# Optimization experiments

Measured on AMD Instinct MI355X. Metric: run time of the kernel, lower is better.

## Reference

```python
import jax, jax.numpy as jnp
import numpy as np
import math

RES = 1024          # FastTrigLookup / FastPhaseProcessor resolution
TWO_PI = 2.0 * math.pi
D = 512             # model dim


def setup_inputs() -> dict:
    key = jax.random.key(0)
    ks = jax.random.split(key, 4)
    B, L = 4, 4096

    def xavier(k, shape):
        fan_out, fan_in = shape
        std = math.sqrt(2.0 / (fan_in + fan_out))
        return jax.random.normal(k, shape, jnp.float32) * std

    return {
        "x": jax.random.normal(ks[0], (B, L, D), jnp.float32),
        "ft_w": xavier(ks[1], (2 * D, D)),
        "ft_b": jnp.zeros((2 * D,), jnp.float32),
        "ln_g": jnp.ones((2 * D,), jnp.float32),
        "ln_b": jnp.zeros((2 * D,), jnp.float32),
        "exc": jnp.ones((1,), jnp.float32) * 0.1,  # excitation_factor init
        "qkv_w": xavier(ks[2], (6 * D, 6 * D)),
        "qkv_b": jnp.zeros((6 * D,), jnp.float32),
        "op_w": xavier(ks[3], (2 * D, 2 * D)),
        "op_b": jnp.zeros((2 * D,), jnp.float32),
    }


def _forward(x, ft_w, ft_b, ln_g, ln_b, exc, qkv_w, qkv_b, op_w, op_b):
    B, L = x.shape[:2]
    sin_tab = jnp.sin(jnp.linspace(0.0, TWO_PI, RES)).astype(x.dtype)
    cos_tab = jnp.cos(jnp.linspace(0.0, TWO_PI, RES)).astype(x.dtype)

    # --- SimpleQuantumState: fused Linear -> tanh-GELU -> LayerNorm ---
    t = x @ ft_w.T + ft_b                                  # [B,L,2D]
    c1, c2 = 0.044715, math.sqrt(2.0 / math.pi)
    g = 0.5 * t * (1.0 + jnp.tanh(c2 * (t + c1 * t ** 3)))
    mu = g.mean(-1, keepdims=True)
    var = ((g - mu) ** 2).mean(-1, keepdims=True)
    n = (g - mu) * jax.lax.rsqrt(var + 1e-5) * ln_g + ln_b
    rp, ip = n[..., :D], n[..., D:]
    # atan2 -> gather-based sin/cos lookup (torch .long() truncates toward 0;
    # negative indices wrap from the end -> emulate with mod RES)
    ang = jnp.arctan2(ip + 1e-8, rp + 1e-8)
    idx = jnp.mod((ang / TWO_PI * (RES - 1)).astype(jnp.int32), RES)
    real = rp * cos_tab[idx]
    imag = ip * sin_tab[idx]
    nrm = jax.lax.rsqrt(real ** 2 + imag ** 2 + 1e-8) * math.sqrt(1.0 / D)
    real, imag = real * nrm, imag * nrm

    # --- EnhancedDynamicPhaseSpace: collapse prevention via trig lookup ---
    amp = jnp.sqrt(real ** 2 + imag ** 2 + 1e-8)
    coll = (amp < 0.1).astype(x.dtype)
    el = jnp.linspace(0.0, 1.0, D) * TWO_PI                # energy_levels * 2pi
    lidx = jnp.clip((jnp.mod(el, TWO_PI) / TWO_PI * RES).astype(jnp.int32), 0, RES - 1)
    real = real + coll * cos_tab[lidx] * exc
    imag = imag + coll * sin_tab[lidx] * exc
    nrm2 = jax.lax.rsqrt(real ** 2 + imag ** 2 + 1e-8)
    real, imag = real * nrm2, imag * nrm2

    # --- BasicQuantumAttention with q=k=v = quantum state (pad_mask=None) ---
    qkv_in = jnp.concatenate([real, imag, real, imag, real, imag], axis=-1)  # [B,L,6D]
    qkv = (qkv_in @ qkv_w.T + qkv_b).reshape(B, L, 6, D)
    q_r, k_r = qkv[:, :, 0], qkv[:, :, 2]
    v_r, v_i = qkv[:, :, 4], qkv[:, :, 5]
    scores = jnp.einsum('bld,bmd->blm', q_r, k_r) * (D ** -0.5)
    attn = jax.nn.softmax(scores, axis=-1)                 # dropout=eval -> identity
    o = jnp.concatenate([jnp.einsum('blm,bmd->bld', attn, v_r),
                         jnp.einsum('blm,bmd->bld', attn, v_i)], axis=-1)
    out = o @ op_w.T + op_b                                # [B,L,2D]
    return out


def reference(x, ft_w, ft_b, ln_g, ln_b, exc, qkv_w, qkv_b, op_w, op_b):
    out = _forward(x, ft_w, ft_b, ln_g, ln_b, exc, qkv_w, qkv_b, op_w, op_b)
    return (out[..., :D], out[..., D:])
```

## Files before the change

### kernel.cpp

```cpp
#include <hip/hip_runtime.h>
#include <hip/hip_bf16.h>
#include <math.h>


#define TWO_PI_F 6.283185307179586f

typedef __attribute__((ext_vector_type(4))) float f32x4;
typedef __attribute__((ext_vector_type(8))) short bf16x8;
typedef __attribute__((ext_vector_type(4))) unsigned short u16x4;
typedef __hip_bfloat16 bf16;

__device__ __forceinline__ void gl_lds16(const void* g, void* l) {
  __builtin_amdgcn_global_load_lds((const __attribute__((address_space(1))) void*)g,
                                   (__attribute__((address_space(3))) void*)l, 16, 0, 0);
}
__device__ __forceinline__ unsigned short f2bf_bits(float f) {
  union { __hip_bfloat16 h; unsigned short u; } cv;
  cv.h = __float2bfloat16(f);
  return cv.u;
}
__device__ __forceinline__ float bf_bits2f(unsigned short b) {
  union { unsigned int u; float f; } cv;
  cv.u = ((unsigned int)b) << 16;
  return cv.f;
}

template <int EPI, int ORD>
__global__ __launch_bounds__(256, 2) void gemm128(
    const bf16* __restrict__ A, const bf16* __restrict__ B, void* __restrict__ C,
    void* __restrict__ Cx, const float* __restrict__ bias, int K, int lda, int ldb, int ldc,
    float scale, long long zsa, long long zsb, long long zsc, float* __restrict__ P0,
    float* __restrict__ P1) {
  __shared__ __align__(16) bf16 sA[128 * 64];
  __shared__ __align__(16) bf16 sB[128 * 64];
  const int tid = threadIdx.x;
  const int lane = tid & 63, wid = tid >> 6;
  const int wm = wid >> 1, wn = wid & 1;

  const int gx = gridDim.x, gy = gridDim.y;
  int flat = blockIdx.x + gx * (blockIdx.y + gy * blockIdx.z);
  {
    const int nwg = gx * gy * gridDim.z;
    const int q = nwg >> 3, r = nwg & 7;
    const int x = flat & 7, loc = flat >> 3;
    flat = (x < r ? x * (q + 1) : r * (q + 1) + (x - r) * q) + loc;
  }
  const int bx = flat % gx;
  const int by = (flat / gx) % gy;
  const int bz = flat / (gx * gy);
  const int bm = by * 128, bn = bx * 128;

  const bf16 *Az, *Bz;
  if constexpr (EPI == 3) {
    const int b = bz & 1, c = bz >> 1;
    Az = A + (long long)b * zsa + c * 2048;
    Bz = B + (long long)b * zsb + c * 2048;
  } else {
    Az = A + (long long)bz * zsa;
    Bz = B + (long long)bz * zsb;
  }

  f32x4 acc[4][4];
#pragma unroll
  for (int i = 0; i < 4; ++i)
#pragma unroll
    for (int j = 0; j < 4; ++j) acc[i][j] = (f32x4){0.f, 0.f, 0.f, 0.f};

  int rowStg[4], gaStg[4];
#pragma unroll
  for (int t = 0; t < 4; ++t) {
    const int c = tid + 256 * t;
    const int r = c >> 3, s = c & 7;
    rowStg[t] = r;
    gaStg[t] = ((s ^ (r & 7)) << 3);
  }
  long long rowA[4], rowB[4];
#pragma unroll
  for (int t = 0; t < 4; ++t) {
    rowA[t] = (long long)(bm + rowStg[t]) * lda + gaStg[t];
    rowB[t] = (long long)(bn + rowStg[t]) * ldb + gaStg[t];
  }

  const int fr = lane & 15, ksl = lane >> 4;

  for (int k0 = 0; k0 < K; k0 += 64) {
#pragma unroll
    for (int t = 0; t < 4; ++t)
      gl_lds16(Az + rowA[t] + k0, &sA[(tid + 256 * t) * 8]);
#pragma unroll
    for (int t = 0; t < 4; ++t)
      gl_lds16(Bz + rowB[t] + k0, &sB[(tid + 256 * t) * 8]);
    __syncthreads();
    bf16x8 af[4][2], bfv[4][2];
#pragma unroll
    for (int i = 0; i < 4; ++i) {
      const int R = wm * 64 + i * 16 + fr;
#pragma unroll
      for (int kk = 0; kk < 2; ++kk) {
        const int s = (kk * 4 + ksl) ^ (R & 7);
        af[i][kk] = *(const bf16x8*)&sA[R * 64 + s * 8];
      }
    }
#pragma unroll
    for (int j = 0; j < 4; ++j) {
      const int R = wn * 64 + j * 16 + fr;
#pragma unroll
      for (int kk = 0; kk < 2; ++kk) {
        const int s = (kk * 4 + ksl) ^ (R & 7);
        bfv[j][kk] = *(const bf16x8*)&sB[R * 64 + s * 8];
      }
    }
#pragma unroll
    for (int kk = 0; kk < 2; ++kk)
#pragma unroll
      for (int i = 0; i < 4; ++i)
#pragma unroll
        for (int j = 0; j < 4; ++j) {
          if constexpr (ORD == 0)
            acc[i][j] =
                __builtin_amdgcn_mfma_f32_16x16x32_bf16(af[i][kk], bfv[j][kk], acc[i][j], 0, 0, 0);
          else
            acc[i][j] =
                __builtin_amdgcn_mfma_f32_16x16x32_bf16(bfv[j][kk], af[i][kk], acc[i][j], 0, 0, 0);
        }
    __syncthreads();
  }

#pragma unroll
  for (int i = 0; i < 4; ++i)
#pragma unroll
    for (int j = 0; j < 4; ++j) {
      if constexpr (ORD == 1) {
        const int row = bm + wm * 64 + i * 16 + fr;
        const int col0 = bn + wn * 64 + j * 16 + ksl * 4;
        f32x4 v = acc[i][j];
#pragma unroll
        for (int r = 0; r < 4; ++r) v[r] *= scale;
        if constexpr (EPI == 0 || EPI == 1) {
          if (bias) {
            const f32x4 bv = *(const f32x4*)&bias[col0];
            v += bv;
          }
        }
        if constexpr (EPI == 1) {
#pragma unroll
          for (int r = 0; r < 4; ++r) {
            const float t = v[r];
            float y = 0.7978845608028654f * (t + 0.044715f * t * t * t);
            y = fminf(fmaxf(y, -15.f), 15.f);
            const float e = __expf(2.f * y);
            v[r] = t * e / (1.f + e);
          }
        }
        if constexpr (EPI == 3) {
          const int b = bz & 1, c = bz >> 1;
          if (c == 0) {
            const f32x4 bv = *(const f32x4*)&bias[col0];
            v += bv;
            float* dst = (col0 < 512) ? (float*)C : (float*)Cx;
            const long long rout = zsc + (long long)b * 4096 + row;
            *(f32x4*)&dst[rout * 512 + (col0 & 511)] = v;
          } else {
            float* dst = b ? P1 : P0;
            *(f32x4*)&dst[(long long)row * 1024 + col0] = v;
          }
        } else if constexpr (EPI == 2) {
          bf16* cc = (bf16*)C + (long long)bz * zsc;
          u16x4 w;
#pragma unroll
          for (int r = 0; r < 4; ++r) w[r] = f2bf_bits(v[r]);
          *(u16x4*)&cc[(long long)row * ldc + col0] = w;
        } else {
          bf16* cc = (bf16*)C;
          u16x4 w;
#pragma unroll
          for (int r = 0; r < 4; ++r) w[r] = f2bf_bits(v[r]);
          *(u16x4*)&cc[(long long)row * ldc + col0] = w;
        }
      } else {
        const int row0 = bm + wm * 64 + i * 16 + ksl * 4;
        const int d = bn + wn * 64 + j * 16 + fr;
        u16x4 w;
#pragma unroll
        for (int r = 0; r < 4; ++r) w[r] = f2bf_bits(acc[i][j][r] * scale + bias[d]);
        const int b = row0 >> 12, mm = row0 & 4095;
        *(u16x4*)((unsigned short*)Cx + ((long long)(b * 1024 + d)) * 4096 + mm) = w;
      }
    }
  (void)ldc;
}

__global__ __launch_bounds__(256) void combine_kernel(const float* __restrict__ p0,
                                                      const float* __restrict__ p1,
                                                      float* __restrict__ out0,
                                                      float* __restrict__ out1) {
  const int idx = blockIdx.x * 256 + threadIdx.x;
  const int b = idx >> 20;
  const int rem = idx & 1048575;
  const int row = rem >> 8;
  const int c4 = rem & 255;
  const float* p = b ? p1 : p0;
  const f32x4 v = *(const f32x4*)(p + (long long)row * 1024 + c4 * 4);
  float* dst = (c4 < 128) ? out0 : out1;
  const long long o = ((long long)(b * 4096 + row)) * 512 + (c4 & 127) * 4;
  f32x4 d = *(f32x4*)(dst + o);
  d += v;
  *(f32x4*)(dst + o) = d;
}

__global__ __launch_bounds__(256) void ln_phase_kernel(
    const bf16* __restrict__ g, bf16* __restrict__ u, const float* __restrict__ ln_g,
    const float* __restrict__ ln_b, const float* __restrict__ lcos,
    const float* __restrict__ lsin, const float* __restrict__ cost,
    const float* __restrict__ sint) {
  __shared__ float sg[1024];
  __shared__ float red[4];
  const int tid = threadIdx.x;
  const int lane = tid & 63, wid = tid >> 6;
  const long long row = blockIdx.x;
  const bf16* gr = g + row * 1024;

  const u16x4 raw = *(const u16x4*)(gr + tid * 4);
  float lv[4];
  float lsum = 0.f;
#pragma unroll
  for (int e = 0; e < 4; ++e) {
    lv[e] = bf_bits2f(raw[e]);
    lsum += lv[e];
  }
  *(f32x4*)&sg[tid * 4] = *(f32x4*)lv;
#pragma unroll
  for (int off = 32; off > 0; off >>= 1) lsum += __shfl_xor(lsum, off);
  if (lane == 0) red[wid] = lsum;
  __syncthreads();
  const float mu = (red[0] + red[1] + red[2] + red[3]) * (1.0f / 1024.0f);
  __syncthreads();
  float lvar = 0.f;
#pragma unroll
  for (int e = 0; e < 4; ++e) {
    const float d = lv[e] - mu;
    lvar += d * d;
  }
#pragma unroll
  for (int off = 32; off > 0; off >>= 1) lvar += __shfl_xor(lvar, off);
  if (lane == 0) red[wid] = lvar;
  __syncthreads();
  const float var = (red[0] + red[1] + red[2] + red[3]) * (1.0f / 1024.0f);
  const float rs = rsqrtf(var + 1e-5f);

#pragma unroll
  for (int kk = 0; kk < 2; ++kk) {
    const int p = tid + kk * 256;
    const float rp = (sg[p] - mu) * rs * ln_g[p] + ln_b[p];
    const float ip = (sg[p + 512] - mu) * rs * ln_g[p + 512] + ln_b[p + 512];
    const float ang = atan2f(ip + 1e-8f, rp + 1e-8f);
    int idx = (int)((ang / TWO_PI_F) * 1023.0f);
    idx = idx < 0 ? idx + 1024 : idx;
    float real = rp * cost[idx];
    float imag = ip * sint[idx];
    const float nrm = rsqrtf(real * real + imag * imag + 1e-8f) * 0.044194173824159216f;
    real *= nrm;
    imag *= nrm;
    const float amp = sqrtf(real * real + imag * imag + 1e-8f);
    const float coll = (amp < 0.1f) ? 1.0f : 0.0f;
    real += coll * lcos[p];
    imag += coll * lsin[p];
    const float n2 = rsqrtf(real * real + imag * imag + 1e-8f);
    u[row * 1024 + p] = __float2bfloat16(real * n2);
    u[row * 1024 + 512 + p] = __float2bfloat16(imag * n2);
  }
}

__global__ __launch_bounds__(256) void softmax_kernel(bf16* __restrict__ s) {
  __shared__ float ss[4096];
  __shared__ float red[4];
  const int tid = threadIdx.x;
  const int lane = tid & 63, wid = tid >> 6;
  bf16* sr = s + (long long)blockIdx.x * 4096;
  float mx = -3.0e38f;
#pragma unroll
  for (int k = 0; k < 4; ++k) {
    const int base = (k * 256 + tid) * 4;
    const u16x4 raw = *(const u16x4*)(sr + base);
    f32x4 f;
#pragma unroll
    for (int e = 0; e < 4; ++e) {
      f[e] = bf_bits2f(raw[e]);
      mx = fmaxf(mx, f[e]);
    }
    *(f32x4*)&ss[base] = f;
  }
#pragma unroll
  for (int off = 32; off > 0; off >>= 1) mx = fmaxf(mx, __shfl_xor(mx, off));
  if (lane == 0) red[wid] = mx;
  __syncthreads();
  mx = fmaxf(fmaxf(red[0], red[1]), fmaxf(red[2], red[3]));
  __syncthreads();
  float sum = 0.f;
#pragma unroll
  for (int k = 0; k < 4; ++k) {
    const int base = (k * 256 + tid) * 4;
    f32x4 f = *(f32x4*)&ss[base];
#pragma unroll
    for (int e = 0; e < 4; ++e) {
      f[e] = __expf(f[e] - mx);
      sum += f[e];
    }
    *(f32x4*)&ss[base] = f;
  }
#pragma unroll
  for (int off = 32; off > 0; off >>= 1) sum += __shfl_xor(sum, off);
  if (lane == 0) red[wid] = sum;
  __syncthreads();
  const float inv = 1.0f / (red[0] + red[1] + red[2] + red[3]);
#pragma unroll
  for (int k = 0; k < 4; ++k) {
    const int base = (k * 256 + tid) * 4;
    const f32x4 f = *(f32x4*)&ss[base];
    u16x4 w;
#pragma unroll
    for (int e = 0; e < 4; ++e) w[e] = f2bf_bits(f[e] * inv);
    *(u16x4*)(sr + base) = w;
  }
}

__global__ __launch_bounds__(256) void fold_all(
    const float* __restrict__ w, const float* __restrict__ b,
    const float* __restrict__ op_w, const float* __restrict__ exc,
    const float* __restrict__ ft_w, const float* __restrict__ x, bf16* __restrict__ weff,
    bf16* __restrict__ wvT, float* __restrict__ beff, float* __restrict__ cost,
    float* __restrict__ sint, float* __restrict__ lcos, float* __restrict__ lsin,
    bf16* __restrict__ ftw_b, bf16* __restrict__ opw_b, bf16* __restrict__ x_b) {
  __shared__ float tile[32][33];
  __shared__ float red[4];
  const int blk = blockIdx.x;
  const int tid = threadIdx.x;
  if (blk < 4096) {
    const int i = blk * 256 + tid;
    const int o = i >> 10, j = i & 1023;
    const int so = (o < 512) ? o : o + 512;
    const float* wr = w + (long long)so * 3072;
    weff[i] = __float2bfloat16(wr[j] + wr[1024 + j] + wr[2048 + j]);
    if (j == 0) beff[o] = b[so];
  } else if (blk < 5120) {
    const int tb = blk - 4096;
    const int t0 = (tb & 31) * 32, j0 = (tb >> 5) * 32;
    const int tx = tid & 31, ty = tid >> 5;
#pragma unroll
    for (int k = 0; k < 4; ++k) {
      const int t = t0 + ty + k * 8;
      const float* wr = w + (long long)(2048 + t) * 3072 + j0 + tx;
      tile[ty + k * 8][tx] = wr[0] + wr[1024] + wr[2048];
    }
    __syncthreads();
#pragma unroll
    for (int k = 0; k < 4; ++k) {
      const int r = ty + k * 8;
      wvT[(long long)(j0 + r) * 1024 + t0 + tx] = __float2bfloat16(tile[tx][r]);
    }
  } else if (blk < 6144) {
    const int o = blk - 5120;
    const int lane = tid & 63, wid = tid >> 6;
    float s = 0.f;
#pragma unroll
    for (int k = 0; k < 4; ++k) {
      const int t = tid + k * 256;
      s += op_w[(long long)o * 1024 + t] * b[2048 + t];
    }
#pragma unroll
    for (int off = 32; off > 0; off >>= 1) s += __shfl_xor(s, off);
    if (lane == 0) red[wid] = s;
    __syncthreads();
    if (tid == 0) beff[1024 + o] = red[0] + red[1] + red[2] + red[3];
  } else if (blk == 6144) {
    const double step = 6.283185307179586 / 1023.0;
#pragma unroll
    for (int k = 0; k < 4; ++k) {
      const int i = tid + k * 256;
      const float a = (float)((double)i * step);
      cost[i] = cosf(a);
      sint[i] = sinf(a);
    }
#pragma unroll
    for (int k = 0; k < 2; ++k) {
      const int i = tid + k * 256;
      const float el = ((float)i / 511.0f) * TWO_PI_F;
      const float m = fmodf(el, TWO_PI_F);
      int li = (int)((m / TWO_PI_F) * 1024.0f);
      li = min(max(li, 0), 1023);
      const float a = (float)((double)li * step);
      lcos[i] = cosf(a) * exc[0];
      lsin[i] = sinf(a) * exc[0];
    }
  } else if (blk < 6657) {
    const long long q = (long long)(blk - 6145) * 256 + tid;
    const f32x4 f = *(const f32x4*)(ft_w + q * 4);
    u16x4 wv;
#pragma unroll
    for (int e = 0; e < 4; ++e) wv[e] = f2bf_bits(f[e]);
    *(u16x4*)((unsigned short*)ftw_b + q * 4) = wv;
  } else if (blk < 7681) {
    const long long q = (long long)(blk - 6657) * 256 + tid;
    const f32x4 f = *(const f32x4*)(op_w + q * 4);
    u16x4 wv;
#pragma unroll
    for (int e = 0; e < 4; ++e) wv[e] = f2bf_bits(f[e]);
    *(u16x4*)((unsigned short*)opw_b + q * 4) = wv;
  } else {
    const long long q0 = (long long)(blk - 7681) * 256 + tid;
#pragma unroll
    for (int t = 0; t < 4; ++t) {
      const long long q = q0 + (long long)t * 524288;
      const f32x4 f = *(const f32x4*)(x + q * 4);
      u16x4 wv;
#pragma unroll
      for (int e = 0; e < 4; ++e) wv[e] = f2bf_bits(f[e]);
      *(u16x4*)((unsigned short*)x_b + q * 4) = wv;
    }
  }
}

extern "C" void kernel_launch(void* const* d_in, const int* in_sizes, int n_in, void* d_out,
                              int out_size, void* d_ws, size_t ws_size, hipStream_t stream) {
  const float* x = (const float*)d_in[0];
  const float* ft_w = (const float*)d_in[1];
  const float* ft_b = (const float*)d_in[2];
  const float* ln_g = (const float*)d_in[3];
  const float* ln_b = (const float*)d_in[4];
  const float* exc = (const float*)d_in[5];
  const float* qkv_w = (const float*)d_in[6];
  const float* qkv_b = (const float*)d_in[7];
  const float* op_w = (const float*)d_in[8];
  const float* op_b = (const float*)d_in[9];

  char* ws = (char*)d_ws;
  const size_t MB = 1024ull * 1024ull;
  bf16* ftw_b = (bf16*)(ws + 0);
  bf16* weff = (bf16*)(ws + 1 * MB);
  bf16* opw_b = (bf16*)(ws + 5 * MB);
  bf16* wvT = (bf16*)(ws + 7 * MB);
  float* beff = (float*)(ws + 9 * MB);
  float* cost = (float*)(ws + 9 * MB + 8192);
  float* sint = (float*)(ws + 9 * MB + 12288);
  float* lcos = (float*)(ws + 9 * MB + 16384);
  float* lsin = (float*)(ws + 9 * MB + 18432);
  bf16* v2T = (bf16*)(ws + 10 * MB);
  bf16* qk = (bf16*)(ws + 42 * MB);
  bf16* x_b = (bf16*)(ws + 74 * MB);
  bf16* gbuf = (bf16*)(ws + 90 * MB);
  bf16* ubuf = (bf16*)(ws + 122 * MB);
  bf16* sc = (bf16*)(ws + 74 * MB);
  float* part0 = (float*)(ws + 138 * MB);
  float* part1 = (float*)(ws + 154 * MB);

  fold_all<<<9729, 256, 0, stream>>>(qkv_w, qkv_b, op_w, exc, ft_w, x, weff, wvT, beff, cost,
                                     sint, lcos, lsin, ftw_b, opw_b, x_b);

  gemm128<0, 1><<<dim3(8, 8), 256, 0, stream>>>(opw_b, wvT, weff + 1024 * 1024, nullptr,
                                                nullptr, 1024, 1024, 1024, 1024, 1.0f, 0, 0,
                                                0, nullptr, nullptr);
  gemm128<1, 1><<<dim3(8, 128), 256, 0, stream>>>(x_b, ftw_b, gbuf, nullptr, ft_b, 512, 512,
                                                  512, 1024, 1.0f, 0, 0, 0, nullptr, nullptr);
  ln_phase_kernel<<<16384, 256, 0, stream>>>(gbuf, ubuf, ln_g, ln_b, lcos, lsin, cost, sint);
  gemm128<0, 1><<<dim3(8, 128), 256, 0, stream>>>(ubuf, weff, qk, nullptr, beff, 1024, 1024,
                                                  1024, 1024, 1.0f, 0, 0, 0, nullptr, nullptr);
  gemm128<4, 0><<<dim3(8, 128), 256, 0, stream>>>(ubuf, weff + 1024 * 1024, nullptr, v2T,
                                                  beff + 1024, 1024, 1024, 1024, 0, 1.0f, 0,
                                                  0, 0, nullptr, nullptr);

  float* out0 = (float*)d_out;
  float* out1 = out0 + 8388608LL;
  for (int p = 0; p < 2; ++p) {
    const bf16* qbase = qk + (long long)(2 * p) * 4096 * 1024;
    gemm128<2, 1><<<dim3(32, 32, 2), 256, 0, stream>>>(
        qbase, qbase + 512, sc, nullptr, nullptr, 512, 1024, 1024, 4096,
        0.04419417382415922f, 4096LL * 1024, 4096LL * 1024, 4096LL * 4096, nullptr, nullptr);
    softmax_kernel<<<8192, 256, 0, stream>>>(sc);
    gemm128<3, 1><<<dim3(8, 32, 4), 256, 0, stream>>>(
        sc, v2T + (long long)(2 * p) * 1024 * 4096, out0, out1, op_b, 2048, 4096, 4096, 0,
        1.0f, 4096LL * 4096, 1024LL * 4096, (long long)(2 * p) * 4096, part0, part1);
    combine_kernel<<<8192, 256, 0, stream>>>(part0, part1,
                                             out0 + (long long)(2 * p) * 4096 * 512,
                                             out1 + (long long)(2 * p) * 4096 * 512);
  }
  (void)in_sizes;
  (void)n_in;
  (void)out_size;
  (void)ws_size;
}
```

Before: 483.7 us.

## Batch attention across all batches when workspace allows, drop split-K combine

When the workspace is large enough, all four batches' score GEMMs and softmax run in one launch each. The attention-times-V GEMM then runs with full K=4096 and writes the bias-added output directly. This removes the split-K partial buffers and the combine kernel. The old split-K epilogue is kept as EPI 5 for the small-workspace fallback. Softmax also keeps its row in registers instead of LDS, which avoids shared-memory round trips but raises register use.

```diff
diff --git a/kernel.cpp b/kernel.cpp
--- a/kernel.cpp
+++ b/kernel.cpp
@@ -51,7 +51,7 @@
   const int bm = by * 128, bn = bx * 128;
 
   const bf16 *Az, *Bz;
-  if constexpr (EPI == 3) {
+  if constexpr (EPI == 5) {
     const int b = bz & 1, c = bz >> 1;
     Az = A + (long long)b * zsa + c * 2048;
     Bz = B + (long long)b * zsb + c * 2048;
@@ -66,30 +66,23 @@
 #pragma unroll
     for (int j = 0; j < 4; ++j) acc[i][j] = (f32x4){0.f, 0.f, 0.f, 0.f};
 
-  int rowStg[4], gaStg[4];
+  long long rowA[4], rowB[4];
 #pragma unroll
   for (int t = 0; t < 4; ++t) {
     const int c = tid + 256 * t;
     const int r = c >> 3, s = c & 7;
-    rowStg[t] = r;
-    gaStg[t] = ((s ^ (r & 7)) << 3);
-  }
-  long long rowA[4], rowB[4];
-#pragma unroll
-  for (int t = 0; t < 4; ++t) {
-    rowA[t] = (long long)(bm + rowStg[t]) * lda + gaStg[t];
-    rowB[t] = (long long)(bn + rowStg[t]) * ldb + gaStg[t];
+    const int ga = ((s ^ (r & 7)) << 3);
+    rowA[t] = (long long)(bm + r) * lda + ga;
+    rowB[t] = (long long)(bn + r) * ldb + ga;
   }
 
   const int fr = lane & 15, ksl = lane >> 4;
 
   for (int k0 = 0; k0 < K; k0 += 64) {
 #pragma unroll
-    for (int t = 0; t < 4; ++t)
-      gl_lds16(Az + rowA[t] + k0, &sA[(tid + 256 * t) * 8]);
-#pragma unroll
-    for (int t = 0; t < 4; ++t)
-      gl_lds16(Bz + rowB[t] + k0, &sB[(tid + 256 * t) * 8]);
+    for (int t = 0; t < 4; ++t) gl_lds16(Az + rowA[t] + k0, &sA[(tid + 256 * t) * 8]);
+#pragma unroll
+    for (int t = 0; t < 4; ++t) gl_lds16(Bz + rowB[t] + k0, &sB[(tid + 256 * t) * 8]);
     __syncthreads();
     bf16x8 af[4][2], bfv[4][2];
 #pragma unroll
@@ -153,6 +146,12 @@
           }
         }
         if constexpr (EPI == 3) {
+          const f32x4 bv = *(const f32x4*)&bias[col0];
+          v += bv;
+          float* dst = (col0 < 512) ? (float*)C : (float*)Cx;
+          const long long rout = (long long)bz * 4096 + row;
+          *(f32x4*)&dst[rout * 512 + (col0 & 511)] = v;
+        } else if constexpr (EPI == 5) {
           const int b = bz & 1, c = bz >> 1;
           if (c == 0) {
             const f32x4 bv = *(const f32x4*)&bias[col0];
@@ -272,23 +271,20 @@
 }
 
 __global__ __launch_bounds__(256) void softmax_kernel(bf16* __restrict__ s) {
-  __shared__ float ss[4096];
   __shared__ float red[4];
   const int tid = threadIdx.x;
   const int lane = tid & 63, wid = tid >> 6;
   bf16* sr = s + (long long)blockIdx.x * 4096;
+  f32x4 f[4];
   float mx = -3.0e38f;
 #pragma unroll
   for (int k = 0; k < 4; ++k) {
-    const int base = (k * 256 + tid) * 4;
-    const u16x4 raw = *(const u16x4*)(sr + base);
-    f32x4 f;
+    const u16x4 raw = *(const u16x4*)(sr + (k * 256 + tid) * 4);
 #pragma unroll
     for (int e = 0; e < 4; ++e) {
-      f[e] = bf_bits2f(raw[e]);
-      mx = fmaxf(mx, f[e]);
-    }
-    *(f32x4*)&ss[base] = f;
+      f[k][e] = bf_bits2f(raw[e]);
+      mx = fmaxf(mx, f[k][e]);
+    }
   }
 #pragma unroll
   for (int off = 32; off > 0; off >>= 1) mx = fmaxf(mx, __shfl_xor(mx, off));
@@ -298,16 +294,12 @@
   __syncthreads();
   float sum = 0.f;
 #pragma unroll
-  for (int k = 0; k < 4; ++k) {
-    const int base = (k * 256 + tid) * 4;
-    f32x4 f = *(f32x4*)&ss[base];
+  for (int k = 0; k < 4; ++k)
 #pragma unroll
     for (int e = 0; e < 4; ++e) {
-      f[e] = __expf(f[e] - mx);
-      sum += f[e];
-    }
-    *(f32x4*)&ss[base] = f;
-  }
+      f[k][e] = __expf(f[k][e] - mx);
+      sum += f[k][e];
+    }
 #pragma unroll
   for (int off = 32; off > 0; off >>= 1) sum += __shfl_xor(sum, off);
   if (lane == 0) red[wid] = sum;
@@ -315,12 +307,10 @@
   const float inv = 1.0f / (red[0] + red[1] + red[2] + red[3]);
 #pragma unroll
   for (int k = 0; k < 4; ++k) {
-    const int base = (k * 256 + tid) * 4;
-    const f32x4 f = *(f32x4*)&ss[base];
     u16x4 w;
 #pragma unroll
-    for (int e = 0; e < 4; ++e) w[e] = f2bf_bits(f[e] * inv);
-    *(u16x4*)(sr + base) = w;
+    for (int e = 0; e < 4; ++e) w[e] = f2bf_bits(f[k][e] * inv);
+    *(u16x4*)(sr + (k * 256 + tid) * 4) = w;
   }
 }
 
@@ -453,6 +443,8 @@
   float* part0 = (float*)(ws + 138 * MB);
   float* part1 = (float*)(ws + 154 * MB);
 
+  const bool big = ws_size >= 204 * MB;
+
   fold_all<<<9729, 256, 0, stream>>>(qkv_w, qkv_b, op_w, exc, ft_w, x, weff, wvT, beff, cost,
                                      sint, lcos, lsin, ftw_b, opw_b, x_b);
 
@@ -470,21 +462,31 @@
 
   float* out0 = (float*)d_out;
   float* out1 = out0 + 8388608LL;
-  for (int p = 0; p < 2; ++p) {
-    const bf16* qbase = qk + (long long)(2 * p) * 4096 * 1024;
-    gemm128<2, 1><<<dim3(32, 32, 2), 256, 0, stream>>>(
-        qbase, qbase + 512, sc, nullptr, nullptr, 512, 1024, 1024, 4096,
-        0.04419417382415922f, 4096LL * 1024, 4096LL * 1024, 4096LL * 4096, nullptr, nullptr);
-    softmax_kernel<<<8192, 256, 0, stream>>>(sc);
+  if (big) {
+    gemm128<2, 1><<<dim3(32, 32, 4), 256, 0, stream>>>(
+        qk, qk + 512, sc, nullptr, nullptr, 512, 1024, 1024, 4096, 0.04419417382415922f,
+        4096LL * 1024, 4096LL * 1024, 4096LL * 4096, nullptr, nullptr);
+    softmax_kernel<<<16384, 256, 0, stream>>>(sc);
     gemm128<3, 1><<<dim3(8, 32, 4), 256, 0, stream>>>(
-        sc, v2T + (long long)(2 * p) * 1024 * 4096, out0, out1, op_b, 2048, 4096, 4096, 0,
-        1.0f, 4096LL * 4096, 1024LL * 4096, (long long)(2 * p) * 4096, part0, part1);
-    combine_kernel<<<8192, 256, 0, stream>>>(part0, part1,
-                                             out0 + (long long)(2 * p) * 4096 * 512,
-                                             out1 + (long long)(2 * p) * 4096 * 512);
+        sc, v2T, out0, out1, op_b, 4096, 4096, 4096, 0, 1.0f, 4096LL * 4096, 1024LL * 4096,
+        0, nullptr, nullptr);
+  } else {
+    for (int p = 0; p < 2; ++p) {
+      const bf16* qbase = qk + (long long)(2 * p) * 4096 * 1024;
+      gemm128<2, 1><<<dim3(32, 32, 2), 256, 0, stream>>>(
+          qbase, qbase + 512, sc, nullptr, nullptr, 512, 1024, 1024, 4096,
+          0.04419417382415922f, 4096LL * 1024, 4096LL * 1024, 4096LL * 4096, nullptr,
+          nullptr);
+      softmax_kernel<<<8192, 256, 0, stream>>>(sc);
+      gemm128<5, 1><<<dim3(8, 32, 4), 256, 0, stream>>>(
+          sc, v2T + (long long)(2 * p) * 1024 * 4096, out0, out1, op_b, 2048, 4096, 4096, 0,
+          1.0f, 4096LL * 4096, 1024LL * 4096, (long long)(2 * p) * 4096, part0, part1);
+      combine_kernel<<<8192, 256, 0, stream>>>(part0, part1,
+                                               out0 + (long long)(2 * p) * 4096 * 512,
+                                               out1 + (long long)(2 * p) * 4096 * 512);
+    }
   }
   (void)in_sizes;
   (void)n_in;
   (void)out_size;
-  (void)ws_size;
-}
+}
```

Measured after the change: 433.6 us. 10.4% less time.
